# Kernel optimization log

Measured on AMD Instinct MI355X. Metric: run time of the kernel, lower is better.

Reference implementation:

```python
import jax, jax.numpy as jnp
import numpy as np

LAMB = 1.0
EPS = 1e-16


def setup_inputs() -> dict:
    key = jax.random.key(0)
    kx, km = jax.random.split(key)
    N, D, K = 262144, 128, 64
    x = jax.random.normal(kx, (N, D), dtype=jnp.float32)
    m = jax.random.normal(km, (K, D), dtype=jnp.float32)
    m = m / jnp.linalg.norm(m, axis=1, keepdims=True)  # unit-norm rows like __init__
    return {"x": x, "m": m}


def _entropy(p):
    # replicate torch.where clamping
    p = jnp.where(p <= 0, EPS, p)
    p = jnp.where(p >= 1, 1.0 - EPS, p)
    return -jnp.sum(p * jnp.log(p), axis=-1)


def _p(x, m):
    d2 = (jnp.sum(x * x, axis=-1, keepdims=True)
          - 2.0 * x @ m.T
          + jnp.sum(m * m, axis=-1))  # [N, K]
    return jax.nn.softmax(-d2, axis=-1)


def reference(x, m):
    p = _p(x, m)                      # [N, K]
    intra = jnp.mean(_entropy(p))     # scalar
    mu = jnp.mean(m, axis=0)          # [D]
    p_inter = _p(mu[None, :], m)[0]   # [K]
    inter = _entropy(p_inter)
    total = intra - LAMB * inter
    return (total, intra, inter)
```

## Files before the change

### kernel.cpp

```cpp
#include <hip/hip_runtime.h>
#include <hip/hip_bf16.h>

#define D 128
#define K 64
#define MROW 136

typedef __attribute__((ext_vector_type(8))) short short8;
typedef __attribute__((ext_vector_type(4))) float f32x4;

__device__ inline short f2bf(float f) {
  union { float f; unsigned u; } v; v.f = f;
  unsigned u = v.u;
  return (short)((u + 0x7fffu + ((u >> 16) & 1u)) >> 16);
}

__device__ inline unsigned pk2(float a, float b) {
  union { __hip_bfloat162 h; unsigned u; } c;
  c.h = __float22bfloat162_rn(make_float2(a, b));
  return c.u;
}

__global__ void prep_kernel(const float* __restrict__ m, float* ws) {
  const int j = blockIdx.x;
  const int t = threadIdx.x;
  float a0 = m[j * D + t * 2];
  float a1 = m[j * D + t * 2 + 1];
  short* mb = (short*)(ws + 128);
  mb[j * D + t * 2]     = f2bf(2.0f * a0);
  mb[j * D + t * 2 + 1] = f2bf(2.0f * a1);
  float s = a0 * a0 + a1 * a1;
  for (int off = 1; off < 64; off <<= 1) s += __shfl_xor(s, off, 64);
  if (t == 0) ws[16 + j] = s;
  if (j == 0 && t < 16) ws[t] = 0.0f;
}

__launch_bounds__(256)
__global__ void main_kernel(const float* __restrict__ x, float* ws, int tilesPerWave) {
  __shared__ short ms[64 * MROW];
  const float* mnorm = ws + 16;
  const short* mb = (const short*)(ws + 128);
  const int tid  = threadIdx.x;
  const int lane = tid & 63;
  const int wv   = tid >> 6;
  const int lid  = lane & 15;
  const int quad = lane >> 4;

  const int wave = blockIdx.x * 4 + wv;
  const int base = wave * tilesPerWave;

  f32x4 v[8];
  {
    const float* xb = x + (size_t)(base * 16 + lid) * D + quad * 8;
#pragma unroll
    for (int kk = 0; kk < 4; ++kk) {
      v[2 * kk]     = *(const f32x4*)(xb + kk * 32);
      v[2 * kk + 1] = *(const f32x4*)(xb + kk * 32 + 4);
    }
  }

#pragma unroll
  for (int i = 0; i < 4; ++i) {
    int g = i * 2048 + tid * 8;
    int row = g >> 7, col = g & 127;
    *(short8*)(ms + row * MROW + col) = *(const short8*)(mb + g);
  }
  float mn[4];
#pragma unroll
  for (int jt = 0; jt < 4; ++jt) mn[jt] = mnorm[jt * 16 + lid];
  __syncthreads();

  float hacc = 0.f;

  for (int it = 0; it < tilesPerWave; ++it) {
    short8 a[4];
#pragma unroll
    for (int kk = 0; kk < 4; ++kk) {
      f32x4 v0 = v[2 * kk], v1 = v[2 * kk + 1];
      union { short8 s; unsigned u[4]; } av;
      av.u[0] = pk2(v0[0], v0[1]);
      av.u[1] = pk2(v0[2], v0[3]);
      av.u[2] = pk2(v1[0], v1[1]);
      av.u[3] = pk2(v1[2], v1[3]);
      a[kk] = av.s;
    }

    if (it + 1 < tilesPerWave) {
      const float* xb = x + (size_t)((base + it + 1) * 16 + lid) * D + quad * 8;
#pragma unroll
      for (int kk = 0; kk < 4; ++kk) {
        v[2 * kk]     = *(const f32x4*)(xb + kk * 32);
        v[2 * kk + 1] = *(const f32x4*)(xb + kk * 32 + 4);
      }
    }

    f32x4 acc[4];
#pragma unroll
    for (int jt = 0; jt < 4; ++jt) acc[jt] = (f32x4){0.f, 0.f, 0.f, 0.f};
#pragma unroll
    for (int kk = 0; kk < 4; ++kk) {
#pragma unroll
      for (int jt = 0; jt < 4; ++jt) {
        short8 b = *(const short8*)(ms + (jt * 16 + lid) * MROW + kk * 32 + quad * 8);
        acc[jt] = __builtin_amdgcn_mfma_f32_16x16x32_bf16(a[kk], b, acc[jt], 0, 0, 0);
      }
    }

#pragma unroll
    for (int r = 0; r < 4; ++r) {
      float s0 = acc[0][r] - mn[0];
      float s1 = acc[1][r] - mn[1];
      float s2 = acc[2][r] - mn[2];
      float s3 = acc[3][r] - mn[3];
      float e0 = __expf(s0), e1 = __expf(s1), e2 = __expf(s2), e3 = __expf(s3);
      float S0 = (e0 + e1) + (e2 + e3);
      float S1 = fmaf(s0, e0, fmaf(s1, e1, fmaf(s2, e2, s3 * e3)));
      for (int off = 1; off < 16; off <<= 1) {
        S0 += __shfl_xor(S0, off, 64);
        S1 += __shfl_xor(S1, off, 64);
      }
      float H = __logf(S0) - S1 / S0;
      if (lid == 0) hacc += H;
    }
  }

  for (int off = 1; off < 64; off <<= 1) hacc += __shfl_xor(hacc, off, 64);
  __shared__ float red[4];
  if (lane == 0) red[wv] = hacc;
  __syncthreads();
  if (tid == 0) atomicAdd(ws, red[0] + red[1] + red[2] + red[3]);
}

__global__ void final_kernel(const float* __restrict__ m, const float* ws, float* out, int nRows) {
  __shared__ float mu[D];
  int lane = threadIdx.x;
  for (int d = lane; d < D; d += 64) {
    float s = 0.f;
    for (int j = 0; j < K; ++j) s += m[j * D + d];
    mu[d] = s * (1.0f / K);
  }
  __syncthreads();
  const float* mr = m + lane * D;
  float dot = 0.f;
  for (int d = 0; d < D; ++d) dot += mu[d] * mr[d];
  float s = 2.f * dot - ws[16 + lane];
  float t = s - 20.f;
  float e = __expf(t);
  float S0 = e, S1 = t * e;
  for (int off = 1; off < 64; off <<= 1) {
    S0 += __shfl_xor(S0, off, 64);
    S1 += __shfl_xor(S1, off, 64);
  }
  float inter = __logf(S0) - S1 / S0;
  if (lane == 0) {
    float intra = ws[0] / (float)nRows;
    out[0] = intra - inter;
    out[1] = intra;
    out[2] = inter;
  }
}

extern "C" void kernel_launch(void* const* d_in, const int* in_sizes, int n_in,
                              void* d_out, int out_size, void* d_ws, size_t ws_size,
                              hipStream_t stream) {
  const float* x = (const float*)d_in[0];
  const float* m = (const float*)d_in[1];
  float* ws = (float*)d_ws;
  float* out = (float*)d_out;
  const int N = in_sizes[0] / D;
  const int nTiles16 = N / 16;

  prep_kernel<<<64, 64, 0, stream>>>(m, ws);

  const int blocks = 1024;
  const int tilesPerWave = nTiles16 / (blocks * 4);
  main_kernel<<<blocks, 256, 0, stream>>>(x, ws, tilesPerWave);

  final_kernel<<<1, 64, 0, stream>>>(m, ws, out, N);
}
```

Before: 211.1 us.

## Keep B fragments in registers, reduce rows with DPP, rebalance grid

The centroid bf16 fragments are loaded once per lane into registers, replacing the LDS staging buffer and the per-iteration LDS reads. The 16-lane softmax sums now use DPP row rotations instead of shuffles. The grid becomes 768 blocks with a hardcoded uneven split of 5 or 6 tiles per wave, which spreads the 16x128 x-tiles evenly over the CUs. Next-tile loads are interleaved with MFMA issue. The hardcoded tile split assumes N=262144 and raises register pressure.

Measured after the change: 212.8 us. No clear change (+0.8%).

```diff
diff --git a/kernel.cpp b/kernel.cpp
--- a/kernel.cpp
+++ b/kernel.cpp
@@ -3,7 +3,6 @@
 
 #define D 128
 #define K 64
-#define MROW 136
 
 typedef __attribute__((ext_vector_type(8))) short short8;
 typedef __attribute__((ext_vector_type(4))) float f32x4;
@@ -18,6 +17,19 @@
   union { __hip_bfloat162 h; unsigned u; } c;
   c.h = __float22bfloat162_rn(make_float2(a, b));
   return c.u;
+}
+
+template<int CTRL>
+__device__ inline float dpp_add(float v) {
+  int r = __builtin_amdgcn_update_dpp(0, __float_as_int(v), CTRL, 0xf, 0xf, true);
+  return v + __int_as_float(r);
+}
+__device__ inline float row16_allsum(float v) {
+  v = dpp_add<0x121>(v);
+  v = dpp_add<0x122>(v);
+  v = dpp_add<0x124>(v);
+  v = dpp_add<0x128>(v);
+  return v;
 }
 
 __global__ void prep_kernel(const float* __restrict__ m, float* ws) {
@@ -35,8 +47,7 @@
 }
 
 __launch_bounds__(256)
-__global__ void main_kernel(const float* __restrict__ x, float* ws, int tilesPerWave) {
-  __shared__ short ms[64 * MROW];
+__global__ void main_kernel(const float* __restrict__ x, float* ws) {
   const float* mnorm = ws + 16;
   const short* mb = (const short*)(ws + 128);
   const int tid  = threadIdx.x;
@@ -46,7 +57,8 @@
   const int quad = lane >> 4;
 
   const int wave = blockIdx.x * 4 + wv;
-  const int base = wave * tilesPerWave;
+  const int cnt  = 5 + (wave < 1024 ? 1 : 0);
+  const int base = wave * 5 + (wave < 1024 ? wave : 1024);
 
   f32x4 v[8];
   {
@@ -58,21 +70,26 @@
     }
   }
 
-#pragma unroll
-  for (int i = 0; i < 4; ++i) {
-    int g = i * 2048 + tid * 8;
-    int row = g >> 7, col = g & 127;
-    *(short8*)(ms + row * MROW + col) = *(const short8*)(mb + g);
-  }
+  short8 bfr[4][4];
   float mn[4];
 #pragma unroll
-  for (int jt = 0; jt < 4; ++jt) mn[jt] = mnorm[jt * 16 + lid];
-  __syncthreads();
+  for (int jt = 0; jt < 4; ++jt) {
+    mn[jt] = mnorm[jt * 16 + lid];
+#pragma unroll
+    for (int kk = 0; kk < 4; ++kk)
+      bfr[jt][kk] = *(const short8*)(mb + (jt * 16 + lid) * D + kk * 32 + quad * 8);
+  }
 
   float hacc = 0.f;
 
-  for (int it = 0; it < tilesPerWave; ++it) {
-    short8 a[4];
+  for (int it = 0; it < cnt; ++it) {
+    const bool more = (it + 1 < cnt);
+    const float* xn = x + (size_t)((base + it + 1) * 16 + lid) * D + quad * 8;
+
+    f32x4 acc[4];
+#pragma unroll
+    for (int jt = 0; jt < 4; ++jt) acc[jt] = (f32x4){0.f, 0.f, 0.f, 0.f};
+
 #pragma unroll
     for (int kk = 0; kk < 4; ++kk) {
       f32x4 v0 = v[2 * kk], v1 = v[2 * kk + 1];
@@ -81,28 +98,13 @@
       av.u[1] = pk2(v0[2], v0[3]);
       av.u[2] = pk2(v1[0], v1[1]);
       av.u[3] = pk2(v1[2], v1[3]);
-      a[kk] = av.s;
-    }
-
-    if (it + 1 < tilesPerWave) {
-      const float* xb = x + (size_t)((base + it + 1) * 16 + lid) * D + quad * 8;
+      if (more) {
+        v[2 * kk]     = *(const f32x4*)(xn + kk * 32);
+        v[2 * kk + 1] = *(const f32x4*)(xn + kk * 32 + 4);
+      }
 #pragma unroll
-      for (int kk = 0; kk < 4; ++kk) {
-        v[2 * kk]     = *(const f32x4*)(xb + kk * 32);
-        v[2 * kk + 1] = *(const f32x4*)(xb + kk * 32 + 4);
-      }
-    }
-
-    f32x4 acc[4];
-#pragma unroll
-    for (int jt = 0; jt < 4; ++jt) acc[jt] = (f32x4){0.f, 0.f, 0.f, 0.f};
-#pragma unroll
-    for (int kk = 0; kk < 4; ++kk) {
-#pragma unroll
-      for (int jt = 0; jt < 4; ++jt) {
-        short8 b = *(const short8*)(ms + (jt * 16 + lid) * MROW + kk * 32 + quad * 8);
-        acc[jt] = __builtin_amdgcn_mfma_f32_16x16x32_bf16(a[kk], b, acc[jt], 0, 0, 0);
-      }
+      for (int jt = 0; jt < 4; ++jt)
+        acc[jt] = __builtin_amdgcn_mfma_f32_16x16x32_bf16(av.s, bfr[jt][kk], acc[jt], 0, 0, 0);
     }
 
 #pragma unroll
@@ -114,10 +116,8 @@
       float e0 = __expf(s0), e1 = __expf(s1), e2 = __expf(s2), e3 = __expf(s3);
       float S0 = (e0 + e1) + (e2 + e3);
       float S1 = fmaf(s0, e0, fmaf(s1, e1, fmaf(s2, e2, s3 * e3)));
-      for (int off = 1; off < 16; off <<= 1) {
-        S0 += __shfl_xor(S0, off, 64);
-        S1 += __shfl_xor(S1, off, 64);
-      }
+      S0 = row16_allsum(S0);
+      S1 = row16_allsum(S1);
       float H = __logf(S0) - S1 / S0;
       if (lid == 0) hacc += H;
     }
@@ -167,13 +167,10 @@
   float* ws = (float*)d_ws;
   float* out = (float*)d_out;
   const int N = in_sizes[0] / D;
-  const int nTiles16 = N / 16;
 
   prep_kernel<<<64, 64, 0, stream>>>(m, ws);
 
-  const int blocks = 1024;
-  const int tilesPerWave = nTiles16 / (blocks * 4);
-  main_kernel<<<blocks, 256, 0, stream>>>(x, ws, tilesPerWave);
+  main_kernel<<<768, 256, 0, stream>>>(x, ws);
 
   final_kernel<<<1, 64, 0, stream>>>(m, ws, out, N);
 }
```
